# Kernel optimization log

Measured on AMD Instinct MI355X. Metric: run time of the kernel, lower is better.

## Reference

```python
import jax, jax.numpy as jnp
import numpy as np

D_MODEL = 1024
H = 16
D_HEAD = 64  # d_q = d_k = d_v
B = 2
S = 2048


def setup_inputs() -> dict:
    key = jax.random.key(0)
    ks = jax.random.split(key, 12)
    scale = 1.0 / np.sqrt(D_MODEL)
    inp = {
        "q": jax.random.normal(ks[0], (B, S, D_MODEL), dtype=jnp.float32),
        "k": jax.random.normal(ks[1], (B, S, D_MODEL), dtype=jnp.float32),
        "v": jax.random.normal(ks[2], (B, S, D_MODEL), dtype=jnp.float32),
        "mask": jax.random.uniform(ks[3], (S, S), dtype=jnp.float32),
        # stacked per-head projection weights: [H, d_model, d_head]
        "W_q": jax.random.normal(ks[4], (H, D_MODEL, D_HEAD), dtype=jnp.float32) * scale,
        "b_q": jnp.zeros((H, D_HEAD), dtype=jnp.float32),
        "W_k": jax.random.normal(ks[5], (H, D_MODEL, D_HEAD), dtype=jnp.float32) * scale,
        "b_k": jnp.zeros((H, D_HEAD), dtype=jnp.float32),
        "W_v": jax.random.normal(ks[6], (H, D_MODEL, D_HEAD), dtype=jnp.float32) * scale,
        "b_v": jnp.zeros((H, D_HEAD), dtype=jnp.float32),
        # output projection: [H*d_v, d_model]
        "W_o": jax.random.normal(ks[7], (H * D_HEAD, D_MODEL), dtype=jnp.float32) * (1.0 / np.sqrt(H * D_HEAD)),
        "b_o": jnp.zeros((D_MODEL,), dtype=jnp.float32),
    }
    return inp


def reference(q, k, v, mask, W_q, b_q, W_k, b_k, W_v, b_v, W_o, b_o):
    # Batched QKV projections over all heads (original loops per head).
    Q = jnp.einsum("bsd,hde->bhse", q, W_q) + b_q[None, :, None, :]  # [B,H,S,Dh]
    K = jnp.einsum("bsd,hde->bhse", k, W_k) + b_k[None, :, None, :]
    V = jnp.einsum("bsd,hde->bhse", v, W_v) + b_v[None, :, None, :]
    scale = 1.0 / jnp.sqrt(jnp.asarray(D_HEAD, dtype=Q.dtype))
    # NOTE: mask is MULTIPLICATIVE on the scaled scores (as in the original).
    scores = jnp.einsum("bhse,bhte->bhst", Q, K) * scale * mask  # [B,H,S,S]
    attn = jax.nn.softmax(scores, axis=-1)
    heads = jnp.einsum("bhst,bhte->bhse", attn, V)  # [B,H,S,Dh]
    # concat heads along feature dim (head order matches torch cat order)
    concat = jnp.transpose(heads, (0, 2, 1, 3)).reshape(B, S, H * D_HEAD)
    return concat @ W_o + b_o
```

## Files before the change

kernel.cpp:

```cpp
#include <hip/hip_runtime.h>
#include <stdint.h>

#define DM 1024
#define HNUM 16
#define DH 64
#define BB 2
#define SSEQ 2048

typedef unsigned short ushort_t;
typedef __attribute__((ext_vector_type(8))) short bf16x8;
typedef __attribute__((ext_vector_type(4))) float f32x4;
typedef __attribute__((ext_vector_type(16))) float f32x16;

#define SCALE2 0.18033688011112042f
#define DEFER_THR 11.0f

__device__ __forceinline__ ushort_t f2bf(float f) {
  unsigned u = __builtin_bit_cast(unsigned, f);
  u += 0x7FFFu + ((u >> 16) & 1u);
  return (ushort_t)(u >> 16);
}
__device__ __forceinline__ float bf2f(ushort_t h) {
  return __builtin_bit_cast(float, (unsigned)h << 16);
}
__device__ __forceinline__ float fast_exp2(float x) {
#if __has_builtin(__builtin_amdgcn_exp2f)
  return __builtin_amdgcn_exp2f(x);
#else
  return exp2f(x);
#endif
}
__device__ __forceinline__ unsigned cvt_pk_bf16(float lo, float hi) {
  unsigned r;
  asm("v_cvt_pk_bf16_f32 %0, %1, %2" : "=v"(r) : "v"(lo), "v"(hi));
  return r;
}
__device__ __forceinline__ void plane32_swap(unsigned& a, unsigned& b, int hh) {
#if __has_builtin(__builtin_amdgcn_permlane32_swap)
  typedef int v2i __attribute__((ext_vector_type(2)));
  v2i r = __builtin_amdgcn_permlane32_swap((int)a, (int)b, 0, 0);
  a = (unsigned)r.x; b = (unsigned)r.y;
#else
  unsigned sa = (unsigned)__shfl_xor((int)a, 32);
  unsigned sb = (unsigned)__shfl_xor((int)b, 32);
  unsigned na = hh ? sb : a;
  unsigned nb = hh ? b : sa;
  a = na; b = nb;
#endif
}
__device__ __forceinline__ float xhalf_max(float x, int hh) {
  unsigned a = __builtin_bit_cast(unsigned, x), b = a;
  plane32_swap(a, b, hh);
  return fmaxf(__builtin_bit_cast(float, a), __builtin_bit_cast(float, b));
}
__device__ __forceinline__ float xhalf_sum(float x, int hh) {
  unsigned a = __builtin_bit_cast(unsigned, x), b = a;
  plane32_swap(a, b, hh);
  return __builtin_bit_cast(float, a) + __builtin_bit_cast(float, b);
}

typedef const __attribute__((address_space(1))) unsigned int* gas_ptr;
typedef __attribute__((address_space(3))) unsigned int* las_ptr;
__device__ __forceinline__ void gload_lds16(const void* g, void* l) {
  __builtin_amdgcn_global_load_lds((gas_ptr)(uintptr_t)g, (las_ptr)(uintptr_t)l, 16, 0, 0);
}

__global__ void cvt3_f32_bf16(const float* __restrict__ q, const float* __restrict__ k,
                              const float* __restrict__ v,
                              ushort_t* __restrict__ qd, ushort_t* __restrict__ kd,
                              ushort_t* __restrict__ vd) {
  const int z = blockIdx.y;
  const float* src = z == 0 ? q : (z == 1 ? k : v);
  ushort_t* dst    = z == 0 ? qd : (z == 1 ? kd : vd);
  const int idx = blockIdx.x * 256 + threadIdx.x;
  const float4* s4 = (const float4*)src;
  float4 a = s4[idx * 2], c = s4[idx * 2 + 1];
  union { ushort_t h[8]; uint4 u; } o;
  o.h[0] = f2bf(a.x); o.h[1] = f2bf(a.y); o.h[2] = f2bf(a.z); o.h[3] = f2bf(a.w);
  o.h[4] = f2bf(c.x); o.h[5] = f2bf(c.y); o.h[6] = f2bf(c.z); o.h[7] = f2bf(c.w);
  ((uint4*)dst)[idx] = o.u;
}

__global__ void mask_pack(const float* __restrict__ src, ushort_t* __restrict__ dst) {
  const int TG = blockIdx.x;
  const int T = TG >> 6, G = TG & 63;
  const int tid = threadIdx.x;
  #pragma unroll
  for (int i = 0; i < 2; ++i) {
    const int wd = tid * 2 + i;
    const int l = wd & 63, g2 = (wd >> 6) & 3, a = wd >> 8;
    const int q = G * 32 + (l & 31);
    const int t = T * 64 + a * 32 + g2 * 8 + (l >> 5) * 4;
    float4 mv = *(const float4*)(src + (size_t)q * 2048 + t);
    union { ushort_t h4[4]; uint2 u; } pk;
    pk.h4[0] = f2bf(mv.x * SCALE2); pk.h4[1] = f2bf(mv.y * SCALE2);
    pk.h4[2] = f2bf(mv.z * SCALE2); pk.h4[3] = f2bf(mv.w * SCALE2);
    *(uint2*)(dst + (size_t)TG * 2048 + (size_t)wd * 4) = pk.u;
  }
}

__global__ void transpose_cvt3(const float* __restrict__ Wq, const float* __restrict__ Wk,
                               const float* __restrict__ Wv,
                               ushort_t* __restrict__ dq, ushort_t* __restrict__ dk,
                               ushort_t* __restrict__ dv) {
  __shared__ ushort_t T[64][65];
  const int mat = blockIdx.z >> 4, g = blockIdx.z & 15;
  const float* src = (mat == 0 ? Wq : (mat == 1 ? Wk : Wv)) + (size_t)g * 1024 * 64;
  ushort_t* dst    = (mat == 0 ? dq : (mat == 1 ? dk : dv)) + (size_t)g * 1024 * 64;
  const int r0 = blockIdx.y * 64;
  const int tid = threadIdx.x;
  #pragma unroll
  for (int i = 0; i < 16; ++i) {
    int idx = i * 256 + tid;
    int r = idx >> 6, c = idx & 63;
    T[r][c] = f2bf(src[(size_t)(r0 + r) * 64 + c]);
  }
  __syncthreads();
  #pragma unroll
  for (int i = 0; i < 16; ++i) {
    int idx = i * 256 + tid;
    int cc = idx >> 6, rr = idx & 63;
    dst[(size_t)cc * 1024 + r0 + rr] = T[rr][cc];
  }
}

__global__ void transpose_cvt(const float* __restrict__ src, ushort_t* __restrict__ dst, int R, int C) {
  __shared__ ushort_t T[64][65];
  const int r0 = blockIdx.y * 64, c0 = blockIdx.x * 64;
  const int tid = threadIdx.x;
  #pragma unroll
  for (int i = 0; i < 16; ++i) {
    int idx = i * 256 + tid;
    int r = idx >> 6, c = idx & 63;
    T[r][c] = f2bf(src[(size_t)(r0 + r) * C + c0 + c]);
  }
  __syncthreads();
  #pragma unroll
  for (int i = 0; i < 16; ++i) {
    int idx = i * 256 + tid;
    int cc = idx >> 6, rr = idx & 63;
    dst[(size_t)(c0 + cc) * R + r0 + rr] = T[rr][cc];
  }
}

__device__ __forceinline__ void gemm_mainloop_128(const ushort_t* __restrict__ A,
                                                  const ushort_t* __restrict__ Bm,
                                                  f32x4 (&acc)[4][4], int m0, int n0, int l, int w) {
  __shared__ ushort_t As[128 * 64];
  __shared__ ushort_t Bs[128 * 64];
  const int wr = w >> 1, wc = w & 1;
  for (int ks = 0; ks < 16; ++ks) {
    const int k0 = ks * 64;
    #pragma unroll
    for (int it = 0; it < 4; ++it) {
      const int chunk = it * 4 + w;
      const int row = chunk * 8 + (l >> 3);
      const int kc = ((l & 7) * 8) ^ ((row & 7) * 8);
      gload_lds16(A + (size_t)(m0 + row) * 1024 + k0 + kc, (char*)As + chunk * 1024);
      gload_lds16(Bm + (size_t)(n0 + row) * 1024 + k0 + kc, (char*)Bs + chunk * 1024);
    }
    __syncthreads();
    #pragma unroll
    for (int kk = 0; kk < 2; ++kk) {
      bf16x8 af[4], bfr[4];
      #pragma unroll
      for (int mi = 0; mi < 4; ++mi) {
        const int row = wr * 64 + mi * 16 + (l & 15);
        const int kc = (kk * 32 + (l >> 4) * 8) ^ ((row & 7) * 8);
        af[mi] = *(const bf16x8*)(As + row * 64 + kc);
      }
      #pragma unroll
      for (int ni = 0; ni < 4; ++ni) {
        const int row = wc * 64 + ni * 16 + (l & 15);
        const int kc = (kk * 32 + (l >> 4) * 8) ^ ((row & 7) * 8);
        bfr[ni] = *(const bf16x8*)(Bs + row * 64 + kc);
      }
      #pragma unroll
      for (int mi = 0; mi < 4; ++mi)
        #pragma unroll
        for (int ni = 0; ni < 4; ++ni)
          acc[mi][ni] = __builtin_amdgcn_mfma_f32_16x16x32_bf16(af[mi], bfr[ni], acc[mi][ni], 0, 0, 0);
    }
    __syncthreads();
  }
}

__global__ __launch_bounds__(256, 2) void qkv_gemm(
    const ushort_t* __restrict__ qb, const ushort_t* __restrict__ kb, const ushort_t* __restrict__ vb,
    const ushort_t* __restrict__ Wtq, const ushort_t* __restrict__ Wtk, const ushort_t* __restrict__ Wtv,
    const float* __restrict__ bq, const float* __restrict__ bk, const float* __restrict__ bv,
    ushort_t* __restrict__ Qo, ushort_t* __restrict__ Ko, ushort_t* __restrict__ Vto) {
  const int z = blockIdx.z;
  const ushort_t* A  = z == 0 ? qb : (z == 1 ? kb : vb);
  const ushort_t* Bm = z == 0 ? Wtq : (z == 1 ? Wtk : Wtv);
  const float* bias  = z == 0 ? bq : (z == 1 ? bk : bv);
  ushort_t* out      = z == 0 ? Qo : (z == 1 ? Ko : Vto);
  const int m0 = blockIdx.x * 128, n0 = blockIdx.y * 128;
  const int tid = threadIdx.x, l = tid & 63, w = tid >> 6;
  f32x4 acc[4][4] = {};
  gemm_mainloop_128(A, Bm, acc, m0, n0, l, w);
  const int wr = w >> 1, wc = w & 1;
  #pragma unroll
  for (int mi = 0; mi < 4; ++mi) {
    #pragma unroll
    for (int ni = 0; ni < 4; ++ni) {
      const int n = n0 + wc * 64 + ni * 16 + (l & 15);
      const float bb = bias[n];
      const int mbase = m0 + wr * 64 + mi * 16 + ((l >> 4) << 2);
      if (z < 2) {
        #pragma unroll
        for (int i = 0; i < 4; ++i) {
          const int m = mbase + i;
          const size_t o = (((size_t)((m >> 11) * 16 + (n >> 6))) * 2048 + (m & 2047)) * 64 + (n & 63);
          out[o] = f2bf(acc[mi][ni][i] + bb);
        }
      } else {
        union { ushort_t h[4]; uint2 u2; } pk;
        #pragma unroll
        for (int i = 0; i < 4; ++i) pk.h[i] = f2bf(acc[mi][ni][i] + bb);
        const size_t o = (((size_t)((mbase >> 11) * 16 + (n >> 6))) * 64 + (n & 63)) * 2048 + (mbase & 2047);
        *(uint2*)(out + o) = pk.u2;
      }
    }
  }
}

__global__ __launch_bounds__(256, 2) void out_gemm(const ushort_t* __restrict__ A,
                                                   const ushort_t* __restrict__ Bm,
                                                   const float* __restrict__ bias,
                                                   float* __restrict__ out) {
  __shared__ ushort_t As[64 * 64];
  __shared__ ushort_t Bs[128 * 64];
  const int m0 = blockIdx.x * 64, n0 = blockIdx.y * 128;
  const int tid = threadIdx.x, l = tid & 63, w = tid >> 6;
  const int wr = w >> 1, wc = w & 1;
  f32x4 acc[2][4] = {};
  for (int ks = 0; ks < 16; ++ks) {
    const int k0 = ks * 64;
    #pragma unroll
    for (int it = 0; it < 6; ++it) {
      const int chunk = it * 4 + w;
      if (chunk < 8) {
        const int row = chunk * 8 + (l >> 3);
        const int kc = ((l & 7) * 8) ^ ((row & 7) * 8);
        gload_lds16(A + (size_t)(m0 + row) * 1024 + k0 + kc, (char*)As + chunk * 1024);
      } else {
        const int c2 = chunk - 8;
        const int row = c2 * 8 + (l >> 3);
        const int kc = ((l & 7) * 8) ^ ((row & 7) * 8);
        gload_lds16(Bm + (size_t)(n0 + row) * 1024 + k0 + kc, (char*)Bs + c2 * 1024);
      }
    }
    __syncthreads();
    #pragma unroll
    for (int kk = 0; kk < 2; ++kk) {
      bf16x8 af[2], bfr[4];
      #pragma unroll
      for (int mi = 0; mi < 2; ++mi) {
        const int row = wr * 32 + mi * 16 + (l & 15);
        const int kc = (kk * 32 + (l >> 4) * 8) ^ ((row & 7) * 8);
        af[mi] = *(const bf16x8*)(As + row * 64 + kc);
      }
      #pragma unroll
      for (int ni = 0; ni < 4; ++ni) {
        const int row = wc * 64 + ni * 16 + (l & 15);
        const int kc = (kk * 32 + (l >> 4) * 8) ^ ((row & 7) * 8);
        bfr[ni] = *(const bf16x8*)(Bs + row * 64 + kc);
      }
      #pragma unroll
      for (int mi = 0; mi < 2; ++mi)
        #pragma unroll
        for (int ni = 0; ni < 4; ++ni)
          acc[mi][ni] = __builtin_amdgcn_mfma_f32_16x16x32_bf16(af[mi], bfr[ni], acc[mi][ni], 0, 0, 0);
    }
    __syncthreads();
  }
  #pragma unroll
  for (int mi = 0; mi < 2; ++mi) {
    #pragma unroll
    for (int ni = 0; ni < 4; ++ni) {
      const int n = n0 + wc * 64 + ni * 16 + (l & 15);
      const float bb = bias[n];
      const int mbase = m0 + wr * 32 + mi * 16 + ((l >> 4) << 2);
      #pragma unroll
      for (int i = 0; i < 4; ++i)
        out[(size_t)(mbase + i) * 1024 + n] = acc[mi][ni][i] + bb;
    }
  }
}

__device__ __forceinline__ void stage_kv128(const ushort_t* __restrict__ Kb, const ushort_t* __restrict__ Vb,
                                            int t0, ushort_t* ks, ushort_t* vs, int l, int w) {
  #pragma unroll
  for (int i = 0; i < 4; ++i) {
    const int c = i * 4 + w;
    const int r1 = c * 8 + (l >> 3);
    const int cc = ((l & 7) * 8) ^ ((r1 & 7) * 8);
    gload_lds16(Kb + (size_t)(t0 + r1) * 64 + cc, (char*)ks + c * 1024);
  }
  #pragma unroll
  for (int i = 0; i < 4; ++i) {
    const int c = i * 4 + w;
    const int r1 = c * 4 + (l >> 4);
    const int cc = ((l & 15) * 8) ^ ((r1 & 7) * 8);
    gload_lds16(Vb + (size_t)r1 * 2048 + t0 + cc, (char*)vs + c * 1024);
  }
}

__global__ __launch_bounds__(256, 2) void flash_attn(const ushort_t* __restrict__ Q,
                                                     const ushort_t* __restrict__ K,
                                                     const ushort_t* __restrict__ Vt,
                                                     const ushort_t* __restrict__ maskF,
                                                     ushort_t* __restrict__ concat) {
  const int bh = blockIdx.y, b = bh >> 4, h = bh & 15;
  const int tid = threadIdx.x, l = tid & 63, w = tid >> 6;
  const int hh = l >> 5, q_l = l & 31;
  __shared__ ushort_t Ks[2][128 * 64];
  __shared__ ushort_t Vs[2][64 * 128];
  const ushort_t* Qb = Q + (size_t)bh * 2048 * 64;
  const ushort_t* Kb = K + (size_t)bh * 2048 * 64;
  const ushort_t* Vb = Vt + (size_t)bh * 64 * 2048;
  const int qbase = blockIdx.x * 128 + w * 32;
  const int G = qbase >> 5;

  bf16x8 qf[4];
  #pragma unroll
  for (int s = 0; s < 4; ++s)
    qf[s] = *(const bf16x8*)(Qb + (size_t)(qbase + q_l) * 64 + s * 16 + hh * 8);

  float m_run = -1e30f, l_run = 0.f;
  f32x16 po[2] = {};

  stage_kv128(Kb, Vb, 0, Ks[0], Vs[0], l, w);
  int cur = 0;

  for (int t0 = 0; t0 < 2048; t0 += 128) {
    __syncthreads();
    if (t0 + 128 < 2048) stage_kv128(Kb, Vb, t0 + 128, Ks[cur ^ 1], Vs[cur ^ 1], l, w);

    #pragma unroll
    for (int sub = 0; sub < 2; ++sub) {
      const ushort_t* mbase = maskF + (size_t)(((t0 >> 6) + sub) * 64 + G) * 2048;
      uint2 mw[2][4];
      #pragma unroll
      for (int a = 0; a < 2; ++a)
        #pragma unroll
        for (int g2 = 0; g2 < 4; ++g2)
          mw[a][g2] = *(const uint2*)(mbase + (size_t)(((a * 4 + g2) * 64) + l) * 4);

      f32x16 sc[2] = {};
      __builtin_amdgcn_s_setprio(1);
      #pragma unroll
      for (int s = 0; s < 4; ++s) {
        #pragma unroll
        for (int mt = 0; mt < 2; ++mt) {
          const int row = sub * 64 + mt * 32 + q_l;
          const int col = (s * 16 + hh * 8) ^ ((q_l & 7) * 8);
          const bf16x8 kf = *(const bf16x8*)(Ks[cur] + row * 64 + col);
          sc[mt] = __builtin_amdgcn_mfma_f32_32x32x16_bf16(kf, qf[s], sc[mt], 0, 0, 0);
        }
      }
      __builtin_amdgcn_s_setprio(0);

      float tmax = -1e30f;
      #pragma unroll
      for (int a = 0; a < 2; ++a) {
        #pragma unroll
        for (int g2 = 0; g2 < 4; ++g2) {
          const unsigned lo = mw[a][g2].x, hi = mw[a][g2].y;
          float v0 = sc[a][g2 * 4 + 0] * bf2f((ushort_t)lo);
          float v1 = sc[a][g2 * 4 + 1] * bf2f((ushort_t)(lo >> 16));
          float v2 = sc[a][g2 * 4 + 2] * bf2f((ushort_t)hi);
          float v3 = sc[a][g2 * 4 + 3] * bf2f((ushort_t)(hi >> 16));
          sc[a][g2 * 4 + 0] = v0; sc[a][g2 * 4 + 1] = v1;
          sc[a][g2 * 4 + 2] = v2; sc[a][g2 * 4 + 3] = v3;
          tmax = fmaxf(tmax, fmaxf(fmaxf(v0, v1), fmaxf(v2, v3)));
        }
      }
      tmax = xhalf_max(tmax, hh);

      if (!__all(tmax <= m_run + DEFER_THR)) {
        const float mnew = fmaxf(m_run, tmax);
        const float rf = fast_exp2(m_run - mnew);
        m_run = mnew;
        l_run *= rf;
        #pragma unroll
        for (int et = 0; et < 2; ++et)
          #pragma unroll
          for (int r = 0; r < 16; ++r) po[et][r] *= rf;
      }

      float psum = 0.f;
      unsigned pw[2][8];
      #pragma unroll
      for (int a = 0; a < 2; ++a)
        #pragma unroll
        for (int j = 0; j < 8; ++j) {
          const float p0 = fast_exp2(sc[a][2 * j] - m_run);
          const float p1 = fast_exp2(sc[a][2 * j + 1] - m_run);
          psum += p0 + p1;
          pw[a][j] = cvt_pk_bf16(p0, p1);
        }
      l_run += xhalf_sum(psum, hh);

      #pragma unroll
      for (int a = 0; a < 2; ++a) {
        plane32_swap(pw[a][0], pw[a][2], hh);
        plane32_swap(pw[a][1], pw[a][3], hh);
        plane32_swap(pw[a][4], pw[a][6], hh);
        plane32_swap(pw[a][5], pw[a][7], hh);
      }

      __builtin_amdgcn_s_setprio(1);
      #pragma unroll
      for (int s = 0; s < 4; ++s) {
        union { unsigned u[4]; bf16x8 v; } pf;
        pf.u[0] = pw[s >> 1][(s & 1) * 4 + 0];
        pf.u[1] = pw[s >> 1][(s & 1) * 4 + 1];
        pf.u[2] = pw[s >> 1][(s & 1) * 4 + 2];
        pf.u[3] = pw[s >> 1][(s & 1) * 4 + 3];
        #pragma unroll
        for (int et = 0; et < 2; ++et) {
          const int row = et * 32 + q_l;
          const int col = sub * 64 + ((s * 16 + hh * 8) ^ ((q_l & 7) * 8));
          const bf16x8 vf = *(const bf16x8*)(Vs[cur] + row * 128 + col);
          po[et] = __builtin_amdgcn_mfma_f32_32x32x16_bf16(vf, pf.v, po[et], 0, 0, 0);
        }
      }
      __builtin_amdgcn_s_setprio(0);
    }
    cur ^= 1;
  }

  const float invl = 1.0f / l_run;
  __syncthreads();
  ushort_t* ow = &Ks[0][0] + w * 2048;
  #pragma unroll
  for (int et = 0; et < 2; ++et)
    #pragma unroll
    for (int r = 0; r < 16; ++r) {
      const int e = et * 32 + (r & 3) + 8 * (r >> 2) + 4 * hh;
      const int ba = (q_l * 128 + e * 2) ^ ((q_l & 7) << 4);
      *(ushort_t*)((char*)ow + ba) = f2bf(po[et][r] * invl);
    }
  __syncthreads();
  {
    union { ushort_t hs[32]; uint2 u2[8]; uint4 u4[4]; } ov;
    const int ebase = hh * 32;
    #pragma unroll
    for (int c = 0; c < 8; ++c) {
      const int e0 = ebase + c * 4;
      const int ba = (q_l * 128 + e0 * 2) ^ ((q_l & 7) << 4);
      ov.u2[c] = *(const uint2*)((const char*)ow + ba);
    }
    ushort_t* dst = concat + ((size_t)(b * 2048 + qbase + q_l)) * 1024 + h * 64 + ebase;
    #pragma unroll
    for (int c2 = 0; c2 < 4; ++c2)
      ((uint4*)dst)[c2] = ov.u4[c2];
  }
}

extern "C" void kernel_launch(void* const* d_in, const int* in_sizes, int n_in,
                              void* d_out, int out_size, void* d_ws, size_t ws_size,
                              hipStream_t stream) {
  const float* q    = (const float*)d_in[0];
  const float* k    = (const float*)d_in[1];
  const float* v    = (const float*)d_in[2];
  const float* mask = (const float*)d_in[3];
  const float* Wq   = (const float*)d_in[4];
  const float* bq   = (const float*)d_in[5];
  const float* Wk   = (const float*)d_in[6];
  const float* bk   = (const float*)d_in[7];
  const float* Wv   = (const float*)d_in[8];
  const float* bv   = (const float*)d_in[9];
  const float* Wo   = (const float*)d_in[10];
  const float* bo   = (const float*)d_in[11];

  const size_t SZ8M = (size_t)4096 * 1024 * 2;
  const size_t SZ2M = (size_t)1024 * 1024 * 2;
  if (ws_size < 7 * SZ8M + 4 * SZ2M) return;

  char* p = (char*)d_ws;
  ushort_t* qb    = (ushort_t*)p; p += SZ8M;
  ushort_t* kb    = (ushort_t*)p; p += SZ8M;
  ushort_t* vb    = (ushort_t*)p; p += SZ8M;
  ushort_t* maskb = (ushort_t*)p; p += SZ8M;
  ushort_t* Qo    = (ushort_t*)p; p += SZ8M;
  ushort_t* Ko    = (ushort_t*)p; p += SZ8M;
  ushort_t* Vto   = (ushort_t*)p; p += SZ8M;
  ushort_t* Wtq   = (ushort_t*)p; p += SZ2M;
  ushort_t* Wtk   = (ushort_t*)p; p += SZ2M;
  ushort_t* Wtv   = (ushort_t*)p; p += SZ2M;
  ushort_t* Wot   = (ushort_t*)p; p += SZ2M;
  ushort_t* concat = qb;

  cvt3_f32_bf16<<<dim3(2048, 3), dim3(256), 0, stream>>>(q, k, v, qb, kb, vb);
  mask_pack<<<dim3(2048), dim3(256), 0, stream>>>(mask, maskb);
  transpose_cvt3<<<dim3(1, 16, 48), dim3(256), 0, stream>>>(Wq, Wk, Wv, Wtq, Wtk, Wtv);
  transpose_cvt<<<dim3(16, 16), dim3(256), 0, stream>>>(Wo, Wot, 1024, 1024);
  qkv_gemm<<<dim3(32, 8, 3), dim3(256), 0, stream>>>(qb, kb, vb, Wtq, Wtk, Wtv, bq, bk, bv, Qo, Ko, Vto);
  flash_attn<<<dim3(16, 32), dim3(256), 0, stream>>>(Qo, Ko, Vto, maskb, concat);
  out_gemm<<<dim3(64, 8), dim3(256), 0, stream>>>(concat, Wot, bo, (float*)d_out);
}
```

Measured before the change: 144.7 us.

## Shrink flash-attention blocks to two waves and prefetch the mask one tile ahead

Each flash-attention block now has 128 threads covering 64 query rows instead of 256 threads covering 128, so the grid doubles. K/V staging uses 64-key tiles in a manually unrolled double buffer, and LDS use per block is halved. Mask values for the next tile are loaded into registers while the current tile is computed, which hides that global-load latency. The row max and row sum are also reduced with shorter dependency trees. In exchange, each K/V tile is fetched from global or L2 memory by twice as many blocks, and there are more barriers per key processed.

```diff
diff --git a/kernel.cpp b/kernel.cpp
--- a/kernel.cpp
+++ b/kernel.cpp
@@ -289,25 +289,7 @@
   }
 }
 
-__device__ __forceinline__ void stage_kv128(const ushort_t* __restrict__ Kb, const ushort_t* __restrict__ Vb,
-                                            int t0, ushort_t* ks, ushort_t* vs, int l, int w) {
-  #pragma unroll
-  for (int i = 0; i < 4; ++i) {
-    const int c = i * 4 + w;
-    const int r1 = c * 8 + (l >> 3);
-    const int cc = ((l & 7) * 8) ^ ((r1 & 7) * 8);
-    gload_lds16(Kb + (size_t)(t0 + r1) * 64 + cc, (char*)ks + c * 1024);
-  }
-  #pragma unroll
-  for (int i = 0; i < 4; ++i) {
-    const int c = i * 4 + w;
-    const int r1 = c * 4 + (l >> 4);
-    const int cc = ((l & 15) * 8) ^ ((r1 & 7) * 8);
-    gload_lds16(Vb + (size_t)r1 * 2048 + t0 + cc, (char*)vs + c * 1024);
-  }
-}
-
-__global__ __launch_bounds__(256, 2) void flash_attn(const ushort_t* __restrict__ Q,
+__global__ __launch_bounds__(128, 2) void flash_attn(const ushort_t* __restrict__ Q,
                                                      const ushort_t* __restrict__ K,
                                                      const ushort_t* __restrict__ Vt,
                                                      const ushort_t* __restrict__ maskF,
@@ -315,12 +297,12 @@
   const int bh = blockIdx.y, b = bh >> 4, h = bh & 15;
   const int tid = threadIdx.x, l = tid & 63, w = tid >> 6;
   const int hh = l >> 5, q_l = l & 31;
-  __shared__ ushort_t Ks[2][128 * 64];
-  __shared__ ushort_t Vs[2][64 * 128];
+  __shared__ ushort_t Ks[2][64 * 64];
+  __shared__ ushort_t Vs[2][64 * 64];
   const ushort_t* Qb = Q + (size_t)bh * 2048 * 64;
   const ushort_t* Kb = K + (size_t)bh * 2048 * 64;
   const ushort_t* Vb = Vt + (size_t)bh * 64 * 2048;
-  const int qbase = blockIdx.x * 128 + w * 32;
+  const int qbase = blockIdx.x * 64 + w * 32;
   const int G = qbase >> 5;
 
   bf16x8 qf[4];
@@ -331,105 +313,125 @@
   float m_run = -1e30f, l_run = 0.f;
   f32x16 po[2] = {};
 
-  stage_kv128(Kb, Vb, 0, Ks[0], Vs[0], l, w);
-  int cur = 0;
+  auto stage = [&](int t0, ushort_t* ks, ushort_t* vs) {
+    #pragma unroll
+    for (int i = 0; i < 4; ++i) {
+      const int c = i * 2 + w;
+      const int r1 = c * 8 + (l >> 3);
+      const int cc = ((l & 7) * 8) ^ ((r1 & 7) * 8);
+      gload_lds16(Kb + (size_t)(t0 + r1) * 64 + cc, (char*)ks + c * 1024);
+      gload_lds16(Vb + (size_t)r1 * 2048 + t0 + cc, (char*)vs + c * 1024);
+    }
+  };
+  auto loadmask = [&](int t0, uint2 (&mw)[2][4]) {
+    const ushort_t* mbase = maskF + (size_t)((t0 >> 6) * 64 + G) * 2048;
+    #pragma unroll
+    for (int a = 0; a < 2; ++a)
+      #pragma unroll
+      for (int g2 = 0; g2 < 4; ++g2)
+        mw[a][g2] = *(const uint2*)(mbase + (size_t)(((a * 4 + g2) * 64) + l) * 4);
+  };
+  auto compute = [&](const ushort_t* ks, const ushort_t* vs, const uint2 (&mw)[2][4]) {
+    f32x16 sc[2] = {};
+    __builtin_amdgcn_s_setprio(1);
+    #pragma unroll
+    for (int s = 0; s < 4; ++s) {
+      #pragma unroll
+      for (int mt = 0; mt < 2; ++mt) {
+        const int row = mt * 32 + q_l;
+        const int col = (s * 16 + hh * 8) ^ ((q_l & 7) * 8);
+        const bf16x8 kf = *(const bf16x8*)(ks + row * 64 + col);
+        sc[mt] = __builtin_amdgcn_mfma_f32_32x32x16_bf16(kf, qf[s], sc[mt], 0, 0, 0);
+      }
+    }
+    __builtin_amdgcn_s_setprio(0);
+
+    float gm[8];
+    #pragma unroll
+    for (int a = 0; a < 2; ++a) {
+      #pragma unroll
+      for (int g2 = 0; g2 < 4; ++g2) {
+        const unsigned lo = mw[a][g2].x, hi = mw[a][g2].y;
+        float v0 = sc[a][g2 * 4 + 0] * bf2f((ushort_t)lo);
+        float v1 = sc[a][g2 * 4 + 1] * bf2f((ushort_t)(lo >> 16));
+        float v2 = sc[a][g2 * 4 + 2] * bf2f((ushort_t)hi);
+        float v3 = sc[a][g2 * 4 + 3] * bf2f((ushort_t)(hi >> 16));
+        sc[a][g2 * 4 + 0] = v0; sc[a][g2 * 4 + 1] = v1;
+        sc[a][g2 * 4 + 2] = v2; sc[a][g2 * 4 + 3] = v3;
+        gm[a * 4 + g2] = fmaxf(fmaxf(v0, v1), fmaxf(v2, v3));
+      }
+    }
+    const float x0 = fmaxf(gm[0], gm[1]), x1 = fmaxf(gm[2], gm[3]);
+    const float x2 = fmaxf(gm[4], gm[5]), x3 = fmaxf(gm[6], gm[7]);
+    float tmax = fmaxf(fmaxf(x0, x1), fmaxf(x2, x3));
+    tmax = xhalf_max(tmax, hh);
+
+    if (!__all(tmax <= m_run + DEFER_THR)) {
+      const float mnew = fmaxf(m_run, tmax);
+      const float rf = fast_exp2(m_run - mnew);
+      m_run = mnew;
+      l_run *= rf;
+      #pragma unroll
+      for (int et = 0; et < 2; ++et)
+        #pragma unroll
+        for (int r = 0; r < 16; ++r) po[et][r] *= rf;
+    }
+
+    float ps[4] = {0.f, 0.f, 0.f, 0.f};
+    unsigned pw[2][8];
+    #pragma unroll
+    for (int a = 0; a < 2; ++a)
+      #pragma unroll
+      for (int j = 0; j < 8; ++j) {
+        const float p0 = fast_exp2(sc[a][2 * j] - m_run);
+        const float p1 = fast_exp2(sc[a][2 * j + 1] - m_run);
+        ps[a * 2 + (j & 1)] += p0 + p1;
+        pw[a][j] = cvt_pk_bf16(p0, p1);
+      }
+    l_run += xhalf_sum((ps[0] + ps[1]) + (ps[2] + ps[3]), hh);
+
+    #pragma unroll
+    for (int a = 0; a < 2; ++a) {
+      plane32_swap(pw[a][0], pw[a][2], hh);
+      plane32_swap(pw[a][1], pw[a][3], hh);
+      plane32_swap(pw[a][4], pw[a][6], hh);
+      plane32_swap(pw[a][5], pw[a][7], hh);
+    }
+
+    __builtin_amdgcn_s_setprio(1);
+    #pragma unroll
+    for (int s = 0; s < 4; ++s) {
+      union { unsigned u[4]; bf16x8 v; } pf;
+      pf.u[0] = pw[s >> 1][(s & 1) * 4 + 0];
+      pf.u[1] = pw[s >> 1][(s & 1) * 4 + 1];
+      pf.u[2] = pw[s >> 1][(s & 1) * 4 + 2];
+      pf.u[3] = pw[s >> 1][(s & 1) * 4 + 3];
+      #pragma unroll
+      for (int et = 0; et < 2; ++et) {
+        const int row = et * 32 + q_l;
+        const int col = (s * 16 + hh * 8) ^ ((q_l & 7) * 8);
+        const bf16x8 vf = *(const bf16x8*)(vs + row * 64 + col);
+        po[et] = __builtin_amdgcn_mfma_f32_32x32x16_bf16(vf, pf.v, po[et], 0, 0, 0);
+      }
+    }
+    __builtin_amdgcn_s_setprio(0);
+  };
+
+  stage(0, Ks[0], Vs[0]);
+  uint2 mwA[2][4], mwB[2][4];
+  loadmask(0, mwA);
 
   for (int t0 = 0; t0 < 2048; t0 += 128) {
     __syncthreads();
-    if (t0 + 128 < 2048) stage_kv128(Kb, Vb, t0 + 128, Ks[cur ^ 1], Vs[cur ^ 1], l, w);
-
-    #pragma unroll
-    for (int sub = 0; sub < 2; ++sub) {
-      const ushort_t* mbase = maskF + (size_t)(((t0 >> 6) + sub) * 64 + G) * 2048;
-      uint2 mw[2][4];
-      #pragma unroll
-      for (int a = 0; a < 2; ++a)
-        #pragma unroll
-        for (int g2 = 0; g2 < 4; ++g2)
-          mw[a][g2] = *(const uint2*)(mbase + (size_t)(((a * 4 + g2) * 64) + l) * 4);
-
-      f32x16 sc[2] = {};
-      __builtin_amdgcn_s_setprio(1);
-      #pragma unroll
-      for (int s = 0; s < 4; ++s) {
-        #pragma unroll
-        for (int mt = 0; mt < 2; ++mt) {
-          const int row = sub * 64 + mt * 32 + q_l;
-          const int col = (s * 16 + hh * 8) ^ ((q_l & 7) * 8);
-          const bf16x8 kf = *(const bf16x8*)(Ks[cur] + row * 64 + col);
-          sc[mt] = __builtin_amdgcn_mfma_f32_32x32x16_bf16(kf, qf[s], sc[mt], 0, 0, 0);
-        }
-      }
-      __builtin_amdgcn_s_setprio(0);
-
-      float tmax = -1e30f;
-      #pragma unroll
-      for (int a = 0; a < 2; ++a) {
-        #pragma unroll
-        for (int g2 = 0; g2 < 4; ++g2) {
-          const unsigned lo = mw[a][g2].x, hi = mw[a][g2].y;
-          float v0 = sc[a][g2 * 4 + 0] * bf2f((ushort_t)lo);
-          float v1 = sc[a][g2 * 4 + 1] * bf2f((ushort_t)(lo >> 16));
-          float v2 = sc[a][g2 * 4 + 2] * bf2f((ushort_t)hi);
-          float v3 = sc[a][g2 * 4 + 3] * bf2f((ushort_t)(hi >> 16));
-          sc[a][g2 * 4 + 0] = v0; sc[a][g2 * 4 + 1] = v1;
-          sc[a][g2 * 4 + 2] = v2; sc[a][g2 * 4 + 3] = v3;
-          tmax = fmaxf(tmax, fmaxf(fmaxf(v0, v1), fmaxf(v2, v3)));
-        }
-      }
-      tmax = xhalf_max(tmax, hh);
-
-      if (!__all(tmax <= m_run + DEFER_THR)) {
-        const float mnew = fmaxf(m_run, tmax);
-        const float rf = fast_exp2(m_run - mnew);
-        m_run = mnew;
-        l_run *= rf;
-        #pragma unroll
-        for (int et = 0; et < 2; ++et)
-          #pragma unroll
-          for (int r = 0; r < 16; ++r) po[et][r] *= rf;
-      }
-
-      float psum = 0.f;
-      unsigned pw[2][8];
-      #pragma unroll
-      for (int a = 0; a < 2; ++a)
-        #pragma unroll
-        for (int j = 0; j < 8; ++j) {
-          const float p0 = fast_exp2(sc[a][2 * j] - m_run);
-          const float p1 = fast_exp2(sc[a][2 * j + 1] - m_run);
-          psum += p0 + p1;
-          pw[a][j] = cvt_pk_bf16(p0, p1);
-        }
-      l_run += xhalf_sum(psum, hh);
-
-      #pragma unroll
-      for (int a = 0; a < 2; ++a) {
-        plane32_swap(pw[a][0], pw[a][2], hh);
-        plane32_swap(pw[a][1], pw[a][3], hh);
-        plane32_swap(pw[a][4], pw[a][6], hh);
-        plane32_swap(pw[a][5], pw[a][7], hh);
-      }
-
-      __builtin_amdgcn_s_setprio(1);
-      #pragma unroll
-      for (int s = 0; s < 4; ++s) {
-        union { unsigned u[4]; bf16x8 v; } pf;
-        pf.u[0] = pw[s >> 1][(s & 1) * 4 + 0];
-        pf.u[1] = pw[s >> 1][(s & 1) * 4 + 1];
-        pf.u[2] = pw[s >> 1][(s & 1) * 4 + 2];
-        pf.u[3] = pw[s >> 1][(s & 1) * 4 + 3];
-        #pragma unroll
-        for (int et = 0; et < 2; ++et) {
-          const int row = et * 32 + q_l;
-          const int col = sub * 64 + ((s * 16 + hh * 8) ^ ((q_l & 7) * 8));
-          const bf16x8 vf = *(const bf16x8*)(Vs[cur] + row * 128 + col);
-          po[et] = __builtin_amdgcn_mfma_f32_32x32x16_bf16(vf, pf.v, po[et], 0, 0, 0);
-        }
-      }
-      __builtin_amdgcn_s_setprio(0);
-    }
-    cur ^= 1;
+    stage(t0 + 64, Ks[1], Vs[1]);
+    loadmask(t0 + 64, mwB);
+    compute(Ks[0], Vs[0], mwA);
+    __syncthreads();
+    if (t0 + 128 < 2048) {
+      stage(t0 + 128, Ks[0], Vs[0]);
+      loadmask(t0 + 128, mwA);
+    }
+    compute(Ks[1], Vs[1], mwB);
   }
 
   const float invl = 1.0f / l_run;
@@ -499,6 +501,6 @@
   transpose_cvt3<<<dim3(1, 16, 48), dim3(256), 0, stream>>>(Wq, Wk, Wv, Wtq, Wtk, Wtv);
   transpose_cvt<<<dim3(16, 16), dim3(256), 0, stream>>>(Wo, Wot, 1024, 1024);
   qkv_gemm<<<dim3(32, 8, 3), dim3(256), 0, stream>>>(qb, kb, vb, Wtq, Wtk, Wtv, bq, bk, bv, Qo, Ko, Vto);
-  flash_attn<<<dim3(16, 32), dim3(256), 0, stream>>>(Qo, Ko, Vto, maskb, concat);
+  flash_attn<<<dim3(32, 32), dim3(128), 0, stream>>>(Qo, Ko, Vto, maskb, concat);
   out_gemm<<<dim3(64, 8), dim3(256), 0, stream>>>(concat, Wot, bo, (float*)d_out);
 }
```

New measurement: 141.8 us. -2.0%, faster.

## Fuse prep kernels into one launch and shrink flash-attn KV tile to 64

Applied to the files above, without the earlier changes.

Merges the four preprocessing kernels (activation conversion, mask packing, QKV weight transpose, output weight transpose) into a single launch that dispatches on block index. This removes three kernel launch gaps and their tail effects. The flash attention loop now stages 64-key tiles instead of 128, halving its shared memory, and drops the s_setprio hints. Cross-half reductions now use __shfl_xor instead of permlane32 swaps. The smaller tiles mean twice as many barriers and a shallower prefetch, which may cost attention throughput.

```diff
diff --git a/kernel.cpp b/kernel.cpp
--- a/kernel.cpp
+++ b/kernel.cpp
@@ -48,16 +48,6 @@
   a = na; b = nb;
 #endif
 }
-__device__ __forceinline__ float xhalf_max(float x, int hh) {
-  unsigned a = __builtin_bit_cast(unsigned, x), b = a;
-  plane32_swap(a, b, hh);
-  return fmaxf(__builtin_bit_cast(float, a), __builtin_bit_cast(float, b));
-}
-__device__ __forceinline__ float xhalf_sum(float x, int hh) {
-  unsigned a = __builtin_bit_cast(unsigned, x), b = a;
-  plane32_swap(a, b, hh);
-  return __builtin_bit_cast(float, a) + __builtin_bit_cast(float, b);
-}
 
 typedef const __attribute__((address_space(1))) unsigned int* gas_ptr;
 typedef __attribute__((address_space(3))) unsigned int* las_ptr;
@@ -65,81 +55,78 @@
   __builtin_amdgcn_global_load_lds((gas_ptr)(uintptr_t)g, (las_ptr)(uintptr_t)l, 16, 0, 0);
 }
 
-__global__ void cvt3_f32_bf16(const float* __restrict__ q, const float* __restrict__ k,
-                              const float* __restrict__ v,
-                              ushort_t* __restrict__ qd, ushort_t* __restrict__ kd,
-                              ushort_t* __restrict__ vd) {
-  const int z = blockIdx.y;
-  const float* src = z == 0 ? q : (z == 1 ? k : v);
-  ushort_t* dst    = z == 0 ? qd : (z == 1 ? kd : vd);
-  const int idx = blockIdx.x * 256 + threadIdx.x;
-  const float4* s4 = (const float4*)src;
-  float4 a = s4[idx * 2], c = s4[idx * 2 + 1];
-  union { ushort_t h[8]; uint4 u; } o;
-  o.h[0] = f2bf(a.x); o.h[1] = f2bf(a.y); o.h[2] = f2bf(a.z); o.h[3] = f2bf(a.w);
-  o.h[4] = f2bf(c.x); o.h[5] = f2bf(c.y); o.h[6] = f2bf(c.z); o.h[7] = f2bf(c.w);
-  ((uint4*)dst)[idx] = o.u;
-}
-
-__global__ void mask_pack(const float* __restrict__ src, ushort_t* __restrict__ dst) {
-  const int TG = blockIdx.x;
-  const int T = TG >> 6, G = TG & 63;
-  const int tid = threadIdx.x;
-  #pragma unroll
-  for (int i = 0; i < 2; ++i) {
-    const int wd = tid * 2 + i;
-    const int l = wd & 63, g2 = (wd >> 6) & 3, a = wd >> 8;
-    const int q = G * 32 + (l & 31);
-    const int t = T * 64 + a * 32 + g2 * 8 + (l >> 5) * 4;
-    float4 mv = *(const float4*)(src + (size_t)q * 2048 + t);
-    union { ushort_t h4[4]; uint2 u; } pk;
-    pk.h4[0] = f2bf(mv.x * SCALE2); pk.h4[1] = f2bf(mv.y * SCALE2);
-    pk.h4[2] = f2bf(mv.z * SCALE2); pk.h4[3] = f2bf(mv.w * SCALE2);
-    *(uint2*)(dst + (size_t)TG * 2048 + (size_t)wd * 4) = pk.u;
-  }
-}
-
-__global__ void transpose_cvt3(const float* __restrict__ Wq, const float* __restrict__ Wk,
-                               const float* __restrict__ Wv,
-                               ushort_t* __restrict__ dq, ushort_t* __restrict__ dk,
-                               ushort_t* __restrict__ dv) {
+__global__ void prep_all(const float* __restrict__ q, const float* __restrict__ k,
+                         const float* __restrict__ v, const float* __restrict__ mask,
+                         const float* __restrict__ Wq, const float* __restrict__ Wk,
+                         const float* __restrict__ Wv, const float* __restrict__ Wo,
+                         ushort_t* __restrict__ qd, ushort_t* __restrict__ kd,
+                         ushort_t* __restrict__ vd, ushort_t* __restrict__ maskd,
+                         ushort_t* __restrict__ dq, ushort_t* __restrict__ dk,
+                         ushort_t* __restrict__ dv, ushort_t* __restrict__ dWo) {
   __shared__ ushort_t T[64][65];
-  const int mat = blockIdx.z >> 4, g = blockIdx.z & 15;
-  const float* src = (mat == 0 ? Wq : (mat == 1 ? Wk : Wv)) + (size_t)g * 1024 * 64;
-  ushort_t* dst    = (mat == 0 ? dq : (mat == 1 ? dk : dv)) + (size_t)g * 1024 * 64;
-  const int r0 = blockIdx.y * 64;
-  const int tid = threadIdx.x;
-  #pragma unroll
-  for (int i = 0; i < 16; ++i) {
-    int idx = i * 256 + tid;
-    int r = idx >> 6, c = idx & 63;
-    T[r][c] = f2bf(src[(size_t)(r0 + r) * 64 + c]);
-  }
-  __syncthreads();
-  #pragma unroll
-  for (int i = 0; i < 16; ++i) {
-    int idx = i * 256 + tid;
-    int cc = idx >> 6, rr = idx & 63;
-    dst[(size_t)cc * 1024 + r0 + rr] = T[rr][cc];
-  }
-}
-
-__global__ void transpose_cvt(const float* __restrict__ src, ushort_t* __restrict__ dst, int R, int C) {
-  __shared__ ushort_t T[64][65];
-  const int r0 = blockIdx.y * 64, c0 = blockIdx.x * 64;
-  const int tid = threadIdx.x;
-  #pragma unroll
-  for (int i = 0; i < 16; ++i) {
-    int idx = i * 256 + tid;
-    int r = idx >> 6, c = idx & 63;
-    T[r][c] = f2bf(src[(size_t)(r0 + r) * C + c0 + c]);
-  }
-  __syncthreads();
-  #pragma unroll
-  for (int i = 0; i < 16; ++i) {
-    int idx = i * 256 + tid;
-    int cc = idx >> 6, rr = idx & 63;
-    dst[(size_t)(c0 + cc) * R + r0 + rr] = T[rr][cc];
+  const int bx = blockIdx.x, tid = threadIdx.x;
+  if (bx < 6144) {
+    const int z = bx >> 11, bi = bx & 2047;
+    const float* src = z == 0 ? q : (z == 1 ? k : v);
+    ushort_t* dst    = z == 0 ? qd : (z == 1 ? kd : vd);
+    const int idx = bi * 256 + tid;
+    const float4* s4 = (const float4*)src;
+    float4 a = s4[idx * 2], c = s4[idx * 2 + 1];
+    union { ushort_t h[8]; uint4 u; } o;
+    o.h[0] = f2bf(a.x); o.h[1] = f2bf(a.y); o.h[2] = f2bf(a.z); o.h[3] = f2bf(a.w);
+    o.h[4] = f2bf(c.x); o.h[5] = f2bf(c.y); o.h[6] = f2bf(c.z); o.h[7] = f2bf(c.w);
+    ((uint4*)dst)[idx] = o.u;
+  } else if (bx < 8192) {
+    const int TG = bx - 6144;
+    const int Tt = TG >> 6, G = TG & 63;
+    #pragma unroll
+    for (int i = 0; i < 2; ++i) {
+      const int wd = tid * 2 + i;
+      const int l = wd & 63, g2 = (wd >> 6) & 3, a = wd >> 8;
+      const int qr = G * 32 + (l & 31);
+      const int t = Tt * 64 + a * 32 + g2 * 8 + (l >> 5) * 4;
+      float4 mv = *(const float4*)(mask + (size_t)qr * 2048 + t);
+      union { ushort_t h4[4]; uint2 u; } pk;
+      pk.h4[0] = f2bf(mv.x * SCALE2); pk.h4[1] = f2bf(mv.y * SCALE2);
+      pk.h4[2] = f2bf(mv.z * SCALE2); pk.h4[3] = f2bf(mv.w * SCALE2);
+      *(uint2*)(maskd + (size_t)TG * 2048 + (size_t)wd * 4) = pk.u;
+    }
+  } else if (bx < 8960) {
+    const int id = bx - 8192;
+    const int zz = id >> 4, yy = id & 15;
+    const int mat = zz >> 4, g = zz & 15;
+    const float* src = (mat == 0 ? Wq : (mat == 1 ? Wk : Wv)) + (size_t)g * 1024 * 64;
+    ushort_t* dst    = (mat == 0 ? dq : (mat == 1 ? dk : dv)) + (size_t)g * 1024 * 64;
+    const int r0 = yy * 64;
+    #pragma unroll
+    for (int i = 0; i < 16; ++i) {
+      int idx = i * 256 + tid;
+      int r = idx >> 6, c = idx & 63;
+      T[r][c] = f2bf(src[(size_t)(r0 + r) * 64 + c]);
+    }
+    __syncthreads();
+    #pragma unroll
+    for (int i = 0; i < 16; ++i) {
+      int idx = i * 256 + tid;
+      int cc = idx >> 6, rr = idx & 63;
+      dst[(size_t)cc * 1024 + r0 + rr] = T[rr][cc];
+    }
+  } else {
+    const int id = bx - 8960;
+    const int c0 = (id & 15) * 64, r0 = (id >> 4) * 64;
+    #pragma unroll
+    for (int i = 0; i < 16; ++i) {
+      int idx = i * 256 + tid;
+      int r = idx >> 6, c = idx & 63;
+      T[r][c] = f2bf(Wo[(size_t)(r0 + r) * 1024 + c0 + c]);
+    }
+    __syncthreads();
+    #pragma unroll
+    for (int i = 0; i < 16; ++i) {
+      int idx = i * 256 + tid;
+      int cc = idx >> 6, rr = idx & 63;
+      dWo[(size_t)(c0 + cc) * 1024 + r0 + rr] = T[rr][cc];
+    }
   }
 }
 
@@ -289,20 +276,14 @@
   }
 }
 
-__device__ __forceinline__ void stage_kv128(const ushort_t* __restrict__ Kb, const ushort_t* __restrict__ Vb,
-                                            int t0, ushort_t* ks, ushort_t* vs, int l, int w) {
+__device__ __forceinline__ void stage_kv(const ushort_t* __restrict__ Kb, const ushort_t* __restrict__ Vb,
+                                         int t0, ushort_t* ks, ushort_t* vs, int l, int w) {
   #pragma unroll
-  for (int i = 0; i < 4; ++i) {
-    const int c = i * 4 + w;
+  for (int half = 0; half < 2; ++half) {
+    const int c = half * 4 + w;
     const int r1 = c * 8 + (l >> 3);
     const int cc = ((l & 7) * 8) ^ ((r1 & 7) * 8);
     gload_lds16(Kb + (size_t)(t0 + r1) * 64 + cc, (char*)ks + c * 1024);
-  }
-  #pragma unroll
-  for (int i = 0; i < 4; ++i) {
-    const int c = i * 4 + w;
-    const int r1 = c * 4 + (l >> 4);
-    const int cc = ((l & 15) * 8) ^ ((r1 & 7) * 8);
     gload_lds16(Vb + (size_t)r1 * 2048 + t0 + cc, (char*)vs + c * 1024);
   }
 }
@@ -315,8 +296,8 @@
   const int bh = blockIdx.y, b = bh >> 4, h = bh & 15;
   const int tid = threadIdx.x, l = tid & 63, w = tid >> 6;
   const int hh = l >> 5, q_l = l & 31;
-  __shared__ ushort_t Ks[2][128 * 64];
-  __shared__ ushort_t Vs[2][64 * 128];
+  __shared__ ushort_t Ks[2][64 * 64];
+  __shared__ ushort_t Vs[2][64 * 64];
   const ushort_t* Qb = Q + (size_t)bh * 2048 * 64;
   const ushort_t* Kb = K + (size_t)bh * 2048 * 64;
   const ushort_t* Vb = Vt + (size_t)bh * 64 * 2048;
@@ -331,103 +312,97 @@
   float m_run = -1e30f, l_run = 0.f;
   f32x16 po[2] = {};
 
-  stage_kv128(Kb, Vb, 0, Ks[0], Vs[0], l, w);
+  stage_kv(Kb, Vb, 0, Ks[0], Vs[0], l, w);
   int cur = 0;
 
-  for (int t0 = 0; t0 < 2048; t0 += 128) {
-    __syncthreads();
-    if (t0 + 128 < 2048) stage_kv128(Kb, Vb, t0 + 128, Ks[cur ^ 1], Vs[cur ^ 1], l, w);
-
-    #pragma unroll
-    for (int sub = 0; sub < 2; ++sub) {
-      const ushort_t* mbase = maskF + (size_t)(((t0 >> 6) + sub) * 64 + G) * 2048;
-      uint2 mw[2][4];
-      #pragma unroll
-      for (int a = 0; a < 2; ++a)
+  for (int t0 = 0; t0 < 2048; t0 += 64) {
+    __syncthreads();
+    if (t0 + 64 < 2048) stage_kv(Kb, Vb, t0 + 64, Ks[cur ^ 1], Vs[cur ^ 1], l, w);
+
+    const ushort_t* mbase = maskF + (size_t)((t0 >> 6) * 64 + G) * 2048;
+    uint2 mw[2][4];
+    #pragma unroll
+    for (int a = 0; a < 2; ++a)
+      #pragma unroll
+      for (int g2 = 0; g2 < 4; ++g2)
+        mw[a][g2] = *(const uint2*)(mbase + (size_t)(((a * 4 + g2) * 64) + l) * 4);
+
+    f32x16 sc[2] = {};
+    #pragma unroll
+    for (int s = 0; s < 4; ++s) {
+      #pragma unroll
+      for (int mt = 0; mt < 2; ++mt) {
+        const int row = mt * 32 + q_l;
+        const int col = (s * 16 + hh * 8) ^ ((q_l & 7) * 8);
+        const bf16x8 kf = *(const bf16x8*)(Ks[cur] + row * 64 + col);
+        sc[mt] = __builtin_amdgcn_mfma_f32_32x32x16_bf16(kf, qf[s], sc[mt], 0, 0, 0);
+      }
+    }
+
+    float tmax = -1e30f;
+    #pragma unroll
+    for (int a = 0; a < 2; ++a) {
+      #pragma unroll
+      for (int g2 = 0; g2 < 4; ++g2) {
+        const unsigned lo = mw[a][g2].x, hi = mw[a][g2].y;
+        float v0 = sc[a][g2 * 4 + 0] * bf2f((ushort_t)lo);
+        float v1 = sc[a][g2 * 4 + 1] * bf2f((ushort_t)(lo >> 16));
+        float v2 = sc[a][g2 * 4 + 2] * bf2f((ushort_t)hi);
+        float v3 = sc[a][g2 * 4 + 3] * bf2f((ushort_t)(hi >> 16));
+        sc[a][g2 * 4 + 0] = v0; sc[a][g2 * 4 + 1] = v1;
+        sc[a][g2 * 4 + 2] = v2; sc[a][g2 * 4 + 3] = v3;
+        tmax = fmaxf(tmax, fmaxf(fmaxf(v0, v1), fmaxf(v2, v3)));
+      }
+    }
+    tmax = fmaxf(tmax, __shfl_xor(tmax, 32));
+
+    if (!__all(tmax <= m_run + DEFER_THR)) {
+      const float mnew = fmaxf(m_run, tmax);
+      const float rf = fast_exp2(m_run - mnew);
+      m_run = mnew;
+      l_run *= rf;
+      #pragma unroll
+      for (int et = 0; et < 2; ++et)
         #pragma unroll
-        for (int g2 = 0; g2 < 4; ++g2)
-          mw[a][g2] = *(const uint2*)(mbase + (size_t)(((a * 4 + g2) * 64) + l) * 4);
-
-      f32x16 sc[2] = {};
-      __builtin_amdgcn_s_setprio(1);
-      #pragma unroll
-      for (int s = 0; s < 4; ++s) {
-        #pragma unroll
-        for (int mt = 0; mt < 2; ++mt) {
-          const int row = sub * 64 + mt * 32 + q_l;
-          const int col = (s * 16 + hh * 8) ^ ((q_l & 7) * 8);
-          const bf16x8 kf = *(const bf16x8*)(Ks[cur] + row * 64 + col);
-          sc[mt] = __builtin_amdgcn_mfma_f32_32x32x16_bf16(kf, qf[s], sc[mt], 0, 0, 0);
-        }
-      }
-      __builtin_amdgcn_s_setprio(0);
-
-      float tmax = -1e30f;
-      #pragma unroll
-      for (int a = 0; a < 2; ++a) {
-        #pragma unroll
-        for (int g2 = 0; g2 < 4; ++g2) {
-          const unsigned lo = mw[a][g2].x, hi = mw[a][g2].y;
-          float v0 = sc[a][g2 * 4 + 0] * bf2f((ushort_t)lo);
-          float v1 = sc[a][g2 * 4 + 1] * bf2f((ushort_t)(lo >> 16));
-          float v2 = sc[a][g2 * 4 + 2] * bf2f((ushort_t)hi);
-          float v3 = sc[a][g2 * 4 + 3] * bf2f((ushort_t)(hi >> 16));
-          sc[a][g2 * 4 + 0] = v0; sc[a][g2 * 4 + 1] = v1;
-          sc[a][g2 * 4 + 2] = v2; sc[a][g2 * 4 + 3] = v3;
-          tmax = fmaxf(tmax, fmaxf(fmaxf(v0, v1), fmaxf(v2, v3)));
-        }
-      }
-      tmax = xhalf_max(tmax, hh);
-
-      if (!__all(tmax <= m_run + DEFER_THR)) {
-        const float mnew = fmaxf(m_run, tmax);
-        const float rf = fast_exp2(m_run - mnew);
-        m_run = mnew;
-        l_run *= rf;
-        #pragma unroll
-        for (int et = 0; et < 2; ++et)
-          #pragma unroll
-          for (int r = 0; r < 16; ++r) po[et][r] *= rf;
-      }
-
-      float psum = 0.f;
-      unsigned pw[2][8];
-      #pragma unroll
-      for (int a = 0; a < 2; ++a)
-        #pragma unroll
-        for (int j = 0; j < 8; ++j) {
-          const float p0 = fast_exp2(sc[a][2 * j] - m_run);
-          const float p1 = fast_exp2(sc[a][2 * j + 1] - m_run);
-          psum += p0 + p1;
-          pw[a][j] = cvt_pk_bf16(p0, p1);
-        }
-      l_run += xhalf_sum(psum, hh);
-
-      #pragma unroll
-      for (int a = 0; a < 2; ++a) {
-        plane32_swap(pw[a][0], pw[a][2], hh);
-        plane32_swap(pw[a][1], pw[a][3], hh);
-        plane32_swap(pw[a][4], pw[a][6], hh);
-        plane32_swap(pw[a][5], pw[a][7], hh);
-      }
-
-      __builtin_amdgcn_s_setprio(1);
-      #pragma unroll
-      for (int s = 0; s < 4; ++s) {
-        union { unsigned u[4]; bf16x8 v; } pf;
-        pf.u[0] = pw[s >> 1][(s & 1) * 4 + 0];
-        pf.u[1] = pw[s >> 1][(s & 1) * 4 + 1];
-        pf.u[2] = pw[s >> 1][(s & 1) * 4 + 2];
-        pf.u[3] = pw[s >> 1][(s & 1) * 4 + 3];
-        #pragma unroll
-        for (int et = 0; et < 2; ++et) {
-          const int row = et * 32 + q_l;
-          const int col = sub * 64 + ((s * 16 + hh * 8) ^ ((q_l & 7) * 8));
-          const bf16x8 vf = *(const bf16x8*)(Vs[cur] + row * 128 + col);
-          po[et] = __builtin_amdgcn_mfma_f32_32x32x16_bf16(vf, pf.v, po[et], 0, 0, 0);
-        }
-      }
-      __builtin_amdgcn_s_setprio(0);
+        for (int r = 0; r < 16; ++r) po[et][r] *= rf;
+    }
+
+    float psum = 0.f;
+    unsigned pw[2][8];
+    #pragma unroll
+    for (int a = 0; a < 2; ++a)
+      #pragma unroll
+      for (int j = 0; j < 8; ++j) {
+        const float p0 = fast_exp2(sc[a][2 * j] - m_run);
+        const float p1 = fast_exp2(sc[a][2 * j + 1] - m_run);
+        psum += p0 + p1;
+        pw[a][j] = cvt_pk_bf16(p0, p1);
+      }
+    psum += __shfl_xor(psum, 32);
+    l_run += psum;
+
+    #pragma unroll
+    for (int a = 0; a < 2; ++a) {
+      plane32_swap(pw[a][0], pw[a][2], hh);
+      plane32_swap(pw[a][1], pw[a][3], hh);
+      plane32_swap(pw[a][4], pw[a][6], hh);
+      plane32_swap(pw[a][5], pw[a][7], hh);
+    }
+
+    #pragma unroll
+    for (int s = 0; s < 4; ++s) {
+      union { unsigned u[4]; bf16x8 v; } pf;
+      pf.u[0] = pw[s >> 1][(s & 1) * 4 + 0];
+      pf.u[1] = pw[s >> 1][(s & 1) * 4 + 1];
+      pf.u[2] = pw[s >> 1][(s & 1) * 4 + 2];
+      pf.u[3] = pw[s >> 1][(s & 1) * 4 + 3];
+      #pragma unroll
+      for (int et = 0; et < 2; ++et) {
+        const int row = et * 32 + q_l;
+        const int col = (s * 16 + hh * 8) ^ ((q_l & 7) * 8);
+        const bf16x8 vf = *(const bf16x8*)(Vs[cur] + row * 64 + col);
+        po[et] = __builtin_amdgcn_mfma_f32_32x32x16_bf16(vf, pf.v, po[et], 0, 0, 0);
+      }
     }
     cur ^= 1;
   }
@@ -494,10 +469,8 @@
   ushort_t* Wot   = (ushort_t*)p; p += SZ2M;
   ushort_t* concat = qb;
 
-  cvt3_f32_bf16<<<dim3(2048, 3), dim3(256), 0, stream>>>(q, k, v, qb, kb, vb);
-  mask_pack<<<dim3(2048), dim3(256), 0, stream>>>(mask, maskb);
-  transpose_cvt3<<<dim3(1, 16, 48), dim3(256), 0, stream>>>(Wq, Wk, Wv, Wtq, Wtk, Wtv);
-  transpose_cvt<<<dim3(16, 16), dim3(256), 0, stream>>>(Wo, Wot, 1024, 1024);
+  prep_all<<<dim3(9216), dim3(256), 0, stream>>>(q, k, v, mask, Wq, Wk, Wv, Wo,
+                                                 qb, kb, vb, maskb, Wtq, Wtk, Wtv, Wot);
   qkv_gemm<<<dim3(32, 8, 3), dim3(256), 0, stream>>>(qb, kb, vb, Wtq, Wtk, Wtv, bq, bk, bv, Qo, Ko, Vto);
   flash_attn<<<dim3(16, 32), dim3(256), 0, stream>>>(Qo, Ko, Vto, maskb, concat);
   out_gemm<<<dim3(64, 8), dim3(256), 0, stream>>>(concat, Wot, bo, (float*)d_out);
```

Result: faster. 135.0 us (-6.7%).
